# Kernel optimization log

Measured on AMD Instinct MI355X. Metric: run time of the kernel, lower is better.

The kernel has to match this reference:

```python
import jax, jax.numpy as jnp
import numpy as np

B, PTS, D = 8, 4096, 256          # batch, points per sample, hidden_size
QT, QR, QO = 3000, 216, 1         # num_queries: pos bins, 72*3 euler bins, openness


def setup_inputs() -> dict:
    key = jax.random.key(0)
    ks = jax.random.split(key, 11)
    N = B * PTS
    w = lambda k, s: jax.random.normal(k, s, jnp.float32) * 0.02
    return {
        "feat": jax.random.normal(ks[0], (N, D), jnp.float32),
        "npoints_in_batch": jnp.full((B,), PTS, jnp.int32),
        "queries_t": w(ks[1], (QT, D)),
        "Wk_t": w(ks[2], (D, D)),
        "Wv_t": w(ks[3], (D, D)),
        "queries_r": w(ks[4], (QR, D)),
        "Wk_r": w(ks[5], (D, D)),
        "Wv_r": w(ks[6], (D, D)),
        "queries_o": w(ks[7], (QO, D)),
        "Wk_o": w(ks[8], (D, D)),
        "Wv_o": w(ks[9], (D, D)),
    }


def _aggregate(feat, seg, queries, Wk, Wv):
    """Ragged cross-attention pooling + sum over feature dim.

    feat: (N, D) all points; seg: (N,) sample id per point.
    Equivalent to, per sample b: sum_d( softmax_n(q K_b^T/sqrt(D)) V_b )[q, d]
    => (B, Q) since sum over d commutes: attn @ V.sum(-1).
    """
    d = feat.shape[-1]
    k = feat @ Wk                                  # (N, D)
    vsum = (feat @ Wv).sum(-1)                     # (N,)  row-sum of values
    scores = (k @ queries.T) / jnp.sqrt(jnp.float32(d))  # (N, Q)
    m = jax.ops.segment_max(scores, seg, num_segments=B)  # (B, Q)
    e = jnp.exp(scores - m[seg])                   # (N, Q)
    denom = jax.ops.segment_sum(e, seg, num_segments=B)   # (B, Q)
    numer = jax.ops.segment_sum(e * vsum[:, None], seg, num_segments=B)
    return numer / denom                           # (B, Q)


def reference(feat, npoints_in_batch, queries_t, Wk_t, Wv_t,
              queries_r, Wk_r, Wv_r, queries_o, Wk_o, Wv_o):
    N = feat.shape[0]
    seg = jnp.repeat(jnp.arange(B, dtype=jnp.int32), npoints_in_batch,
                     total_repeat_length=N)
    xt = _aggregate(feat, seg, queries_t, Wk_t, Wv_t)  # (B, 3000)
    xr = _aggregate(feat, seg, queries_r, Wk_r, Wv_r)  # (B, 216)
    xo = _aggregate(feat, seg, queries_o, Wk_o, Wv_o)  # (B, 1)
    return (xt, xr, xo)
```

## Files before the change

### kernel.cpp

```cpp
#include <hip/hip_runtime.h>

typedef __attribute__((ext_vector_type(8))) short short8;
typedef __attribute__((ext_vector_type(4))) float f32x4;
typedef unsigned int u32;

#define D_ 256
#define QT_V 3000
#define QR_V 216
#define QO_V 1
#define QPT 3008
#define QPR 224
#define QPO 96
#define QPTOT 3328
#define WQ_TILES 104
#define NSPLIT 16
#define VPAD 32
#define SCALE 0.09016844005556021f
#define TILE_US 8192
#define PSTRIDE 264

__device__ __forceinline__ unsigned short f2bf(float f) {
    union { float f; unsigned int i; } u; u.f = f;
    unsigned int i = u.i + 0x7fffu + ((u.i >> 16) & 1u);
    return (unsigned short)(i >> 16);
}

__device__ __forceinline__ void async_cp16(const unsigned short* g, unsigned short* l) {
    __builtin_amdgcn_global_load_lds((const __attribute__((address_space(1))) u32*)g,
                                     (__attribute__((address_space(3))) u32*)l, 16, 0, 0);
}

__global__ __launch_bounds__(256) void prep(
    const float* __restrict__ feat,
    const float* __restrict__ q_t, const float* __restrict__ q_r,
    const float* __restrict__ q_o,
    const float* __restrict__ wk_t, const float* __restrict__ wk_r,
    const float* __restrict__ wk_o,
    const float* __restrict__ wv_t, const float* __restrict__ wv_r,
    const float* __restrict__ wv_o,
    unsigned short* __restrict__ featb,
    unsigned short* __restrict__ WqT,
    float* __restrict__ vsum,
    int N, int ntiles, int nvs)
{
    __shared__ __align__(16) unsigned short lds[32 * PSTRIDE];
    int blk = blockIdx.x, tid = (int)threadIdx.x;
    int srow = tid >> 3, c8 = tid & 7;
    int wave = tid >> 6, lane = tid & 63;
    int col16 = lane & 15, quad = lane >> 4;

    if (blk < ntiles) {
        int t = blk;
        int row = t * 32 + srow;
        bool valid = row < N;
#pragma unroll
        for (int i = 0; i < 8; ++i) {
            int col = i * 32 + c8 * 4;
            float4 v;
            if (valid) v = *(const float4*)(feat + (size_t)row * D_ + col);
            else { v.x = v.y = v.z = v.w = 0.f; }
            ushort4 o;
            o.x = f2bf(v.x); o.y = f2bf(v.y); o.z = f2bf(v.z); o.w = f2bf(v.w);
            *(ushort4*)(lds + srow * PSTRIDE + col) = o;
        }
        __syncthreads();
#pragma unroll
        for (int i = 0; i < 4; ++i) {
            int cmb = wave * 4 + i;
            int kk = cmb >> 1, sub = cmb & 1;
            short8 v = *(const short8*)(lds + (sub * 16 + col16) * PSTRIDE
                                        + quad * 8 + kk * 32);
            *(short8*)(featb + (size_t)t * TILE_US + cmb * 512 + lane * 8) = v;
        }
    } else if (blk < ntiles + WQ_TILES) {
        int wq = blk - ntiles;
        const float* Q; const float* Wh; int nvalid, lq0, outrow;
        if (wq < 94)       { Q = q_t; Wh = wk_t; nvalid = QT_V; lq0 = wq * 32;         outrow = lq0; }
        else if (wq < 101) { Q = q_r; Wh = wk_r; nvalid = QR_V; lq0 = (wq - 94) * 32;  outrow = QPT + lq0; }
        else               { Q = q_o; Wh = wk_o; nvalid = QO_V; lq0 = (wq - 101) * 32; outrow = QPT + QPR + lq0; }
        int row = lq0 + srow;
        bool valid = row < nvalid;
#pragma unroll
        for (int i = 0; i < 8; ++i) {
            int col = i * 32 + c8 * 4;
            float4 v;
            if (valid) v = *(const float4*)(Q + (size_t)row * D_ + col);
            else { v.x = v.y = v.z = v.w = 0.f; }
            ushort4 o;
            o.x = f2bf(v.x); o.y = f2bf(v.y); o.z = f2bf(v.z); o.w = f2bf(v.w);
            *(ushort4*)(lds + srow * PSTRIDE + col) = o;
        }
        __syncthreads();
        int c0 = wave * 64;
        f32x4 acc[2][4];
#pragma unroll
        for (int mt = 0; mt < 2; ++mt)
#pragma unroll
            for (int nt = 0; nt < 4; ++nt)
                acc[mt][nt] = f32x4{0.f, 0.f, 0.f, 0.f};
#pragma unroll
        for (int kk = 0; kk < 8; ++kk) {
            short8 a0 = *(const short8*)(lds + col16 * PSTRIDE + quad * 8 + kk * 32);
            short8 a1 = *(const short8*)(lds + (16 + col16) * PSTRIDE + quad * 8 + kk * 32);
#pragma unroll
            for (int nt = 0; nt < 4; ++nt) {
                const float* wr = Wh + (size_t)(c0 + nt * 16 + col16) * D_ + quad * 8 + kk * 32;
                float4 x = *(const float4*)(wr);
                float4 y = *(const float4*)(wr + 4);
                short8 bf;
                bf[0] = (short)f2bf(x.x); bf[1] = (short)f2bf(x.y);
                bf[2] = (short)f2bf(x.z); bf[3] = (short)f2bf(x.w);
                bf[4] = (short)f2bf(y.x); bf[5] = (short)f2bf(y.y);
                bf[6] = (short)f2bf(y.z); bf[7] = (short)f2bf(y.w);
                acc[0][nt] = __builtin_amdgcn_mfma_f32_16x16x32_bf16(a0, bf, acc[0][nt], 0, 0, 0);
                acc[1][nt] = __builtin_amdgcn_mfma_f32_16x16x32_bf16(a1, bf, acc[1][nt], 0, 0, 0);
            }
        }
#pragma unroll
        for (int mt = 0; mt < 2; ++mt)
#pragma unroll
            for (int nt = 0; nt < 4; ++nt)
#pragma unroll
                for (int r = 0; r < 4; ++r) {
                    int orow = outrow + mt * 16 + quad * 4 + r;
                    int ocol = c0 + nt * 16 + col16;
                    WqT[(size_t)orow * D_ + ocol] = f2bf(acc[mt][nt][r] * SCALE);
                }
    } else {
        int v = blk - ntiles - WQ_TILES;
        float* wv = (float*)lds;
        for (int f0 = wave * 4; f0 < 768; f0 += 16) {
            int f = f0 + (lane >> 4);
            int hh = f >> 8, c = f & 255;
            const float* base = ((hh == 0) ? wv_t : (hh == 1) ? wv_r : wv_o)
                                + (size_t)c * D_;
            float s = 0.f;
#pragma unroll
            for (int p = 0; p < 4; ++p) {
                float4 x = *(const float4*)(base + p * 64 + (lane & 15) * 4);
                s += x.x + x.y + x.z + x.w;
            }
            s += __shfl_xor(s, 1); s += __shfl_xor(s, 2);
            s += __shfl_xor(s, 4); s += __shfl_xor(s, 8);
            if ((lane & 15) == 0) wv[f] = s;
        }
        __syncthreads();
        int r0 = v * 128;
#pragma unroll 1
        for (int pass = 0; pass < 32; ++pass) {
            int row = r0 + pass * 4 + wave;
            if (row < N) {
                float4 fv = *(const float4*)(feat + (size_t)row * D_ + lane * 4);
                float4 w0 = *(const float4*)(wv + lane * 4);
                float4 w1 = *(const float4*)(wv + 256 + lane * 4);
                float4 w2 = *(const float4*)(wv + 512 + lane * 4);
                float p0 = fv.x * w0.x + fv.y * w0.y + fv.z * w0.z + fv.w * w0.w;
                float p1 = fv.x * w1.x + fv.y * w1.y + fv.z * w1.z + fv.w * w1.w;
                float p2 = fv.x * w2.x + fv.y * w2.y + fv.z * w2.z + fv.w * w2.w;
#pragma unroll
                for (int off = 32; off >= 1; off >>= 1) {
                    p0 += __shfl_xor(p0, off);
                    p1 += __shfl_xor(p1, off);
                    p2 += __shfl_xor(p2, off);
                }
                if (lane == 0) {
                    vsum[0 * (size_t)(N + VPAD) + row] = p0;
                    vsum[1 * (size_t)(N + VPAD) + row] = p1;
                    vsum[2 * (size_t)(N + VPAD) + row] = p2;
                }
            }
        }
        if (v == nvs - 1 && tid < 3 * VPAD) {
            int hh = tid / VPAD, i = tid % VPAD;
            vsum[(size_t)hh * (N + VPAD) + N + i] = 0.f;
        }
    }
}

__global__ __launch_bounds__(256, 4) void attn_main(
    const unsigned short* __restrict__ featb,
    const int* __restrict__ npts,
    const unsigned short* __restrict__ WqT,
    const float* __restrict__ vsum,
    float* __restrict__ partials, int N)
{
    __shared__ __align__(16) unsigned short lds[2][TILE_US];
    int b = blockIdx.z, qblock = blockIdx.y, chunk = blockIdx.x;
    int tid = (int)threadIdx.x;
    int wave = tid >> 6, lane = tid & 63;
    int col = lane & 15, quad = lane >> 4;

    int qp0 = qblock * 128 + wave * 32;
    int h = (qp0 < QPT) ? 0 : ((qp0 < QPT + QPR) ? 1 : 2);
    const float* vs = vsum + (size_t)h * (N + VPAD);

    int start = 0;
#pragma unroll 1
    for (int i = 0; i < b; ++i) start += npts[i];
    int end = start + npts[b];
    if (end > N) end = N;
    if (start < 0) start = 0;
    if (start > end) start = end;
    int bt0 = start >> 5, bt1 = (end + 31) >> 5;
    int ntc = (bt1 - bt0 + NSPLIT - 1) / NSPLIT;
    int ta = bt0 + chunk * ntc;
    int tb = ta + ntc; if (tb > bt1) tb = bt1;

    short8 bfrag[2][8];
#pragma unroll
    for (int qt = 0; qt < 2; ++qt) {
        const unsigned short* wr = WqT + (size_t)(qp0 + qt * 16 + col) * D_ + quad * 8;
#pragma unroll
        for (int kk = 0; kk < 8; ++kk)
            bfrag[qt][kk] = *(const short8*)(wr + kk * 32);
    }

    float den0 = 0.f, num0 = 0.f, den1 = 0.f, num1 = 0.f;
    int p = 0;
    if (ta < tb) {
        const unsigned short* g = featb + (size_t)ta * TILE_US + (wave * 4) * 512 + lane * 8;
#pragma unroll
        for (int i = 0; i < 4; ++i)
            async_cp16(g + i * 512, &lds[0][(wave * 4 + i) * 512]);
    }
#pragma unroll 1
    for (int t = ta; t < tb; ++t) {
        __syncthreads();
        if (t + 1 < tb) {
            const unsigned short* g = featb + (size_t)(t + 1) * TILE_US + (wave * 4) * 512 + lane * 8;
#pragma unroll
            for (int i = 0; i < 4; ++i)
                async_cp16(g + i * 512, &lds[p ^ 1][(wave * 4 + i) * 512]);
        }
        const unsigned short* lp = lds[p];
        f32x4 acc00 = {0.f,0.f,0.f,0.f}, acc01 = {0.f,0.f,0.f,0.f};
        f32x4 acc10 = {0.f,0.f,0.f,0.f}, acc11 = {0.f,0.f,0.f,0.f};
#pragma unroll
        for (int kk = 0; kk < 8; ++kk) {
            short8 a0 = *(const short8*)(lp + (kk * 2 + 0) * 512 + lane * 8);
            short8 a1 = *(const short8*)(lp + (kk * 2 + 1) * 512 + lane * 8);
            acc00 = __builtin_amdgcn_mfma_f32_16x16x32_bf16(a0, bfrag[0][kk], acc00, 0, 0, 0);
            acc10 = __builtin_amdgcn_mfma_f32_16x16x32_bf16(a0, bfrag[1][kk], acc10, 0, 0, 0);
            acc01 = __builtin_amdgcn_mfma_f32_16x16x32_bf16(a1, bfrag[0][kk], acc01, 0, 0, 0);
            acc11 = __builtin_amdgcn_mfma_f32_16x16x32_bf16(a1, bfrag[1][kk], acc11, 0, 0, 0);
        }
        int rb = t * 32 + quad * 4;
        f32x4 v0 = *(const f32x4*)(vs + rb);
        f32x4 v1 = *(const f32x4*)(vs + rb + 16);
        int r0 = t * 32;
        if (r0 >= start && r0 + 32 <= end) {
#pragma unroll
            for (int r = 0; r < 4; ++r) {
                float e00 = __builtin_amdgcn_exp2f(acc00[r]);
                float e01 = __builtin_amdgcn_exp2f(acc01[r]);
                float e10 = __builtin_amdgcn_exp2f(acc10[r]);
                float e11 = __builtin_amdgcn_exp2f(acc11[r]);
                den0 += e00 + e01; num0 += e00 * v0[r] + e01 * v1[r];
                den1 += e10 + e11; num1 += e10 * v0[r] + e11 * v1[r];
            }
        } else {
#pragma unroll
            for (int r = 0; r < 4; ++r) {
                int ra = rb + r, rb2 = rb + 16 + r;
                bool ma = (ra >= start) && (ra < end);
                bool mb = (rb2 >= start) && (rb2 < end);
                float e00 = ma ? __builtin_amdgcn_exp2f(acc00[r]) : 0.f;
                float e01 = mb ? __builtin_amdgcn_exp2f(acc01[r]) : 0.f;
                float e10 = ma ? __builtin_amdgcn_exp2f(acc10[r]) : 0.f;
                float e11 = mb ? __builtin_amdgcn_exp2f(acc11[r]) : 0.f;
                den0 += e00 + e01; num0 += e00 * v0[r] + e01 * v1[r];
                den1 += e10 + e11; num1 += e10 * v0[r] + e11 * v1[r];
            }
        }
        p ^= 1;
    }

    den0 += __shfl_xor(den0, 16); den0 += __shfl_xor(den0, 32);
    num0 += __shfl_xor(num0, 16); num0 += __shfl_xor(num0, 32);
    den1 += __shfl_xor(den1, 16); den1 += __shfl_xor(den1, 32);
    num1 += __shfl_xor(num1, 16); num1 += __shfl_xor(num1, 32);

    if (quad == 0) {
        size_t base = ((size_t)b * QPTOT + (qp0 + col)) * NSPLIT + chunk;
        partials[base * 2]     = den0;
        partials[base * 2 + 1] = num0;
        size_t base1 = base + (size_t)16 * NSPLIT;
        partials[base1 * 2]     = den1;
        partials[base1 * 2 + 1] = num1;
    }
}

__global__ __launch_bounds__(256) void combine_k(
    const float* __restrict__ partials,
    float* __restrict__ out, int Bn)
{
    int gid = blockIdx.x * 256 + threadIdx.x;
    int total = Bn * QPTOT;
    if (gid >= total) return;
    int b = gid / QPTOT, qp = gid - b * QPTOT;
    const float* p = partials + (size_t)gid * NSPLIT * 2;
    float den = 0.f, num = 0.f;
#pragma unroll
    for (int c = 0; c < NSPLIT; ++c) { den += p[c * 2]; num += p[c * 2 + 1]; }
    float val = (den > 0.f) ? (num / den) : 0.f;
    int oidx = -1;
    if (qp < QPT) {
        if (qp < QT_V) oidx = b * QT_V + qp;
    } else if (qp < QPT + QPR) {
        int q = qp - QPT;
        if (q < QR_V) oidx = Bn * QT_V + b * QR_V + q;
    } else {
        int q = qp - QPT - QPR;
        if (q < QO_V) oidx = Bn * (QT_V + QR_V) + b;
    }
    if (oidx >= 0) out[oidx] = val;
}

extern "C" void kernel_launch(void* const* d_in, const int* in_sizes, int n_in,
                              void* d_out, int out_size, void* d_ws, size_t ws_size,
                              hipStream_t stream)
{
    const float* feat = (const float*)d_in[0];
    const int* npts   = (const int*)d_in[1];
    const float* q_t  = (const float*)d_in[2];
    const float* wk_t = (const float*)d_in[3];
    const float* wv_t = (const float*)d_in[4];
    const float* q_r  = (const float*)d_in[5];
    const float* wk_r = (const float*)d_in[6];
    const float* wv_r = (const float*)d_in[7];
    const float* q_o  = (const float*)d_in[8];
    const float* wk_o = (const float*)d_in[9];
    const float* wv_o = (const float*)d_in[10];

    int N  = in_sizes[0] / D_;
    int Bn = in_sizes[1];
    int ntiles = (N + 31) / 32;
    int nvs = (N + 127) / 128;

    char* ws = (char*)d_ws;
    size_t off = 0;
    unsigned short* WqT = (unsigned short*)(ws + off);
    off += (size_t)QPTOT * D_ * sizeof(unsigned short);
    off = (off + 255) & ~(size_t)255;
    unsigned short* featb = (unsigned short*)(ws + off);
    off += (size_t)ntiles * TILE_US * sizeof(unsigned short);
    off = (off + 255) & ~(size_t)255;
    float* vsum = (float*)(ws + off);
    off += (size_t)3 * (N + VPAD) * sizeof(float);
    off = (off + 255) & ~(size_t)255;
    float* partials = (float*)(ws + off);
    off += (size_t)Bn * QPTOT * NSPLIT * 2 * sizeof(float);
    (void)ws_size;

    prep<<<ntiles + WQ_TILES + nvs, 256, 0, stream>>>(
        feat, q_t, q_r, q_o, wk_t, wk_r, wk_o, wv_t, wv_r, wv_o,
        featb, WqT, vsum, N, ntiles, nvs);

    dim3 grid(NSPLIT, QPTOT / 128, Bn);
    attn_main<<<grid, 256, 0, stream>>>(featb, npts, WqT, vsum, partials, N);

    int total = Bn * QPTOT;
    combine_k<<<(total + 255) / 256, 256, 0, stream>>>(partials, (float*)d_out, Bn);
}
```

Baseline: 208.7 us.

## Fuse prep, attention and combine into one persistent cooperative kernel

Merges the three launches into a single cooperative persistent kernel of 1024 blocks that separates its phases with grid syncs and takes work items from atomic counters. The vsum computation is folded into the feature bf16 conversion tile loop, so feat is read once in prep instead of twice. If the cooperative launch fails, the code falls back to four phased launches. The aim is to remove launch gaps and the redundant feat read, at the cost of grid-sync overhead and dynamic scheduling through atomics, and the occupancy of 4 blocks per CU must hold for the cooperative launch to succeed.

Measured after the change: 572.0 us. 2.74x slower.

```diff
diff --git a/kernel.cpp b/kernel.cpp
--- a/kernel.cpp
+++ b/kernel.cpp
@@ -1,4 +1,7 @@
 #include <hip/hip_runtime.h>
+#include <hip/hip_cooperative_groups.h>
+
+namespace cg = cooperative_groups;
 
 typedef __attribute__((ext_vector_type(8))) short short8;
 typedef __attribute__((ext_vector_type(4))) float f32x4;
@@ -12,12 +15,14 @@
 #define QPR 224
 #define QPO 96
 #define QPTOT 3328
+#define NQB 26
 #define WQ_TILES 104
 #define NSPLIT 16
 #define VPAD 32
 #define SCALE 0.09016844005556021f
 #define TILE_US 8192
 #define PSTRIDE 264
+#define GRIDB 1024
 
 __device__ __forceinline__ unsigned short f2bf(float f) {
     union { float f; unsigned int i; } u; u.f = f;
@@ -30,290 +35,300 @@
                                      (__attribute__((address_space(3))) u32*)l, 16, 0, 0);
 }
 
-__global__ __launch_bounds__(256) void prep(
-    const float* __restrict__ feat,
+__global__ __launch_bounds__(256, 4) void fused(
+    const float* __restrict__ feat, const int* __restrict__ npts,
     const float* __restrict__ q_t, const float* __restrict__ q_r,
     const float* __restrict__ q_o,
     const float* __restrict__ wk_t, const float* __restrict__ wk_r,
     const float* __restrict__ wk_o,
     const float* __restrict__ wv_t, const float* __restrict__ wv_r,
     const float* __restrict__ wv_o,
-    unsigned short* __restrict__ featb,
-    unsigned short* __restrict__ WqT,
-    float* __restrict__ vsum,
-    int N, int ntiles, int nvs)
+    unsigned short* __restrict__ featb, unsigned short* __restrict__ WqT,
+    float* __restrict__ wvsum, float* __restrict__ vsum,
+    float* __restrict__ partials, u32* __restrict__ ctr,
+    float* __restrict__ out,
+    int N, int ntiles, int Bn, int phase)
 {
-    __shared__ __align__(16) unsigned short lds[32 * PSTRIDE];
+    __shared__ __align__(16) unsigned short lds[2][TILE_US];
+    __shared__ int wi_sh;
+    unsigned short* plds = &lds[0][0];
+    cg::grid_group gg = cg::this_grid();
+    bool fm = (phase < 0);
+
     int blk = blockIdx.x, tid = (int)threadIdx.x;
     int srow = tid >> 3, c8 = tid & 7;
     int wave = tid >> 6, lane = tid & 63;
     int col16 = lane & 15, quad = lane >> 4;
 
-    if (blk < ntiles) {
-        int t = blk;
-        int row = t * 32 + srow;
-        bool valid = row < N;
-#pragma unroll
-        for (int i = 0; i < 8; ++i) {
-            int col = i * 32 + c8 * 4;
-            float4 v;
-            if (valid) v = *(const float4*)(feat + (size_t)row * D_ + col);
-            else { v.x = v.y = v.z = v.w = 0.f; }
-            ushort4 o;
-            o.x = f2bf(v.x); o.y = f2bf(v.y); o.z = f2bf(v.z); o.w = f2bf(v.w);
-            *(ushort4*)(lds + srow * PSTRIDE + col) = o;
-        }
-        __syncthreads();
-#pragma unroll
-        for (int i = 0; i < 4; ++i) {
-            int cmb = wave * 4 + i;
-            int kk = cmb >> 1, sub = cmb & 1;
-            short8 v = *(const short8*)(lds + (sub * 16 + col16) * PSTRIDE
-                                        + quad * 8 + kk * 32);
-            *(short8*)(featb + (size_t)t * TILE_US + cmb * 512 + lane * 8) = v;
-        }
-    } else if (blk < ntiles + WQ_TILES) {
-        int wq = blk - ntiles;
-        const float* Q; const float* Wh; int nvalid, lq0, outrow;
-        if (wq < 94)       { Q = q_t; Wh = wk_t; nvalid = QT_V; lq0 = wq * 32;         outrow = lq0; }
-        else if (wq < 101) { Q = q_r; Wh = wk_r; nvalid = QR_V; lq0 = (wq - 94) * 32;  outrow = QPT + lq0; }
-        else               { Q = q_o; Wh = wk_o; nvalid = QO_V; lq0 = (wq - 101) * 32; outrow = QPT + QPR + lq0; }
-        int row = lq0 + srow;
-        bool valid = row < nvalid;
-#pragma unroll
-        for (int i = 0; i < 8; ++i) {
-            int col = i * 32 + c8 * 4;
-            float4 v;
-            if (valid) v = *(const float4*)(Q + (size_t)row * D_ + col);
-            else { v.x = v.y = v.z = v.w = 0.f; }
-            ushort4 o;
-            o.x = f2bf(v.x); o.y = f2bf(v.y); o.z = f2bf(v.z); o.w = f2bf(v.w);
-            *(ushort4*)(lds + srow * PSTRIDE + col) = o;
-        }
-        __syncthreads();
-        int c0 = wave * 64;
-        f32x4 acc[2][4];
-#pragma unroll
-        for (int mt = 0; mt < 2; ++mt)
-#pragma unroll
-            for (int nt = 0; nt < 4; ++nt)
-                acc[mt][nt] = f32x4{0.f, 0.f, 0.f, 0.f};
-#pragma unroll
-        for (int kk = 0; kk < 8; ++kk) {
-            short8 a0 = *(const short8*)(lds + col16 * PSTRIDE + quad * 8 + kk * 32);
-            short8 a1 = *(const short8*)(lds + (16 + col16) * PSTRIDE + quad * 8 + kk * 32);
-#pragma unroll
-            for (int nt = 0; nt < 4; ++nt) {
-                const float* wr = Wh + (size_t)(c0 + nt * 16 + col16) * D_ + quad * 8 + kk * 32;
-                float4 x = *(const float4*)(wr);
-                float4 y = *(const float4*)(wr + 4);
-                short8 bf;
-                bf[0] = (short)f2bf(x.x); bf[1] = (short)f2bf(x.y);
-                bf[2] = (short)f2bf(x.z); bf[3] = (short)f2bf(x.w);
-                bf[4] = (short)f2bf(y.x); bf[5] = (short)f2bf(y.y);
-                bf[6] = (short)f2bf(y.z); bf[7] = (short)f2bf(y.w);
-                acc[0][nt] = __builtin_amdgcn_mfma_f32_16x16x32_bf16(a0, bf, acc[0][nt], 0, 0, 0);
-                acc[1][nt] = __builtin_amdgcn_mfma_f32_16x16x32_bf16(a1, bf, acc[1][nt], 0, 0, 0);
-            }
-        }
-#pragma unroll
-        for (int mt = 0; mt < 2; ++mt)
-#pragma unroll
-            for (int nt = 0; nt < 4; ++nt)
-#pragma unroll
-                for (int r = 0; r < 4; ++r) {
-                    int orow = outrow + mt * 16 + quad * 4 + r;
-                    int ocol = c0 + nt * 16 + col16;
-                    WqT[(size_t)orow * D_ + ocol] = f2bf(acc[mt][nt][r] * SCALE);
-                }
-    } else {
-        int v = blk - ntiles - WQ_TILES;
-        float* wv = (float*)lds;
-        for (int f0 = wave * 4; f0 < 768; f0 += 16) {
-            int f = f0 + (lane >> 4);
-            int hh = f >> 8, c = f & 255;
-            const float* base = ((hh == 0) ? wv_t : (hh == 1) ? wv_r : wv_o)
-                                + (size_t)c * D_;
-            float s = 0.f;
-#pragma unroll
-            for (int p = 0; p < 4; ++p) {
-                float4 x = *(const float4*)(base + p * 64 + (lane & 15) * 4);
-                s += x.x + x.y + x.z + x.w;
-            }
-            s += __shfl_xor(s, 1); s += __shfl_xor(s, 2);
-            s += __shfl_xor(s, 4); s += __shfl_xor(s, 8);
-            if ((lane & 15) == 0) wv[f] = s;
-        }
-        __syncthreads();
-        int r0 = v * 128;
-#pragma unroll 1
-        for (int pass = 0; pass < 32; ++pass) {
-            int row = r0 + pass * 4 + wave;
-            if (row < N) {
-                float4 fv = *(const float4*)(feat + (size_t)row * D_ + lane * 4);
-                float4 w0 = *(const float4*)(wv + lane * 4);
-                float4 w1 = *(const float4*)(wv + 256 + lane * 4);
-                float4 w2 = *(const float4*)(wv + 512 + lane * 4);
-                float p0 = fv.x * w0.x + fv.y * w0.y + fv.z * w0.z + fv.w * w0.w;
-                float p1 = fv.x * w1.x + fv.y * w1.y + fv.z * w1.z + fv.w * w1.w;
-                float p2 = fv.x * w2.x + fv.y * w2.y + fv.z * w2.z + fv.w * w2.w;
-#pragma unroll
-                for (int off = 32; off >= 1; off >>= 1) {
-                    p0 += __shfl_xor(p0, off);
-                    p1 += __shfl_xor(p1, off);
-                    p2 += __shfl_xor(p2, off);
-                }
-                if (lane == 0) {
+    if (fm || phase == 0) {
+        if (blk < 3) {
+            const float* Wv = (blk == 0) ? wv_t : ((blk == 1) ? wv_r : wv_o);
+            for (int f0 = wave * 4; f0 < 256; f0 += 16) {
+                int f = f0 + (lane >> 4);
+                const float* base = Wv + (size_t)f * D_;
+                float s = 0.f;
+#pragma unroll
+                for (int p = 0; p < 4; ++p) {
+                    float4 x = *(const float4*)(base + p * 64 + (lane & 15) * 4);
+                    s += x.x + x.y + x.z + x.w;
+                }
+                s += __shfl_xor(s, 1); s += __shfl_xor(s, 2);
+                s += __shfl_xor(s, 4); s += __shfl_xor(s, 8);
+                if ((lane & 15) == 0) wvsum[blk * 256 + f] = s;
+            }
+        } else if (blk == 3) {
+            if (tid < 2) ctr[tid] = 0u;
+            if (tid < 3 * VPAD) {
+                int hh = tid / VPAD, i = tid % VPAD;
+                vsum[(size_t)hh * (N + VPAD) + N + i] = 0.f;
+            }
+        }
+    }
+    if (fm) gg.sync();
+
+    if (fm || phase == 1) {
+        int totB = ntiles + WQ_TILES;
+        for (;;) {
+            if (tid == 0) wi_sh = (int)atomicAdd(&ctr[0], 1u);
+            __syncthreads();
+            int wi = wi_sh;
+            __syncthreads();
+            if (wi >= totB) break;
+            if (wi < ntiles) {
+                int t = wi;
+                int row = t * 32 + srow;
+                bool valid = row < N;
+                float p0 = 0.f, p1 = 0.f, p2 = 0.f;
+#pragma unroll
+                for (int i = 0; i < 8; ++i) {
+                    int col = i * 32 + c8 * 4;
+                    float4 v;
+                    if (valid) v = *(const float4*)(feat + (size_t)row * D_ + col);
+                    else { v.x = v.y = v.z = v.w = 0.f; }
+                    ushort4 o;
+                    o.x = f2bf(v.x); o.y = f2bf(v.y); o.z = f2bf(v.z); o.w = f2bf(v.w);
+                    *(ushort4*)(plds + srow * PSTRIDE + col) = o;
+                    float4 w0 = *(const float4*)(wvsum + col);
+                    float4 w1 = *(const float4*)(wvsum + 256 + col);
+                    float4 w2 = *(const float4*)(wvsum + 512 + col);
+                    p0 += v.x * w0.x + v.y * w0.y + v.z * w0.z + v.w * w0.w;
+                    p1 += v.x * w1.x + v.y * w1.y + v.z * w1.z + v.w * w1.w;
+                    p2 += v.x * w2.x + v.y * w2.y + v.z * w2.z + v.w * w2.w;
+                }
+                p0 += __shfl_xor(p0, 1); p0 += __shfl_xor(p0, 2); p0 += __shfl_xor(p0, 4);
+                p1 += __shfl_xor(p1, 1); p1 += __shfl_xor(p1, 2); p1 += __shfl_xor(p1, 4);
+                p2 += __shfl_xor(p2, 1); p2 += __shfl_xor(p2, 2); p2 += __shfl_xor(p2, 4);
+                if (c8 == 0 && valid) {
                     vsum[0 * (size_t)(N + VPAD) + row] = p0;
                     vsum[1 * (size_t)(N + VPAD) + row] = p1;
                     vsum[2 * (size_t)(N + VPAD) + row] = p2;
                 }
-            }
-        }
-        if (v == nvs - 1 && tid < 3 * VPAD) {
-            int hh = tid / VPAD, i = tid % VPAD;
-            vsum[(size_t)hh * (N + VPAD) + N + i] = 0.f;
-        }
-    }
-}
-
-__global__ __launch_bounds__(256, 4) void attn_main(
-    const unsigned short* __restrict__ featb,
-    const int* __restrict__ npts,
-    const unsigned short* __restrict__ WqT,
-    const float* __restrict__ vsum,
-    float* __restrict__ partials, int N)
-{
-    __shared__ __align__(16) unsigned short lds[2][TILE_US];
-    int b = blockIdx.z, qblock = blockIdx.y, chunk = blockIdx.x;
-    int tid = (int)threadIdx.x;
-    int wave = tid >> 6, lane = tid & 63;
-    int col = lane & 15, quad = lane >> 4;
-
-    int qp0 = qblock * 128 + wave * 32;
-    int h = (qp0 < QPT) ? 0 : ((qp0 < QPT + QPR) ? 1 : 2);
-    const float* vs = vsum + (size_t)h * (N + VPAD);
-
-    int start = 0;
+                __syncthreads();
+#pragma unroll
+                for (int i = 0; i < 4; ++i) {
+                    int cmb = wave * 4 + i;
+                    int kk = cmb >> 1, sub = cmb & 1;
+                    short8 v = *(const short8*)(plds + (sub * 16 + col16) * PSTRIDE
+                                                + quad * 8 + kk * 32);
+                    *(short8*)(featb + (size_t)t * TILE_US + cmb * 512 + lane * 8) = v;
+                }
+            } else {
+                int wq = wi - ntiles;
+                const float* Q; const float* Wh; int nvalid, lq0, outrow;
+                if (wq < 94)       { Q = q_t; Wh = wk_t; nvalid = QT_V; lq0 = wq * 32;         outrow = lq0; }
+                else if (wq < 101) { Q = q_r; Wh = wk_r; nvalid = QR_V; lq0 = (wq - 94) * 32;  outrow = QPT + lq0; }
+                else               { Q = q_o; Wh = wk_o; nvalid = QO_V; lq0 = (wq - 101) * 32; outrow = QPT + QPR + lq0; }
+                int row = lq0 + srow;
+                bool valid = row < nvalid;
+#pragma unroll
+                for (int i = 0; i < 8; ++i) {
+                    int col = i * 32 + c8 * 4;
+                    float4 v;
+                    if (valid) v = *(const float4*)(Q + (size_t)row * D_ + col);
+                    else { v.x = v.y = v.z = v.w = 0.f; }
+                    ushort4 o;
+                    o.x = f2bf(v.x); o.y = f2bf(v.y); o.z = f2bf(v.z); o.w = f2bf(v.w);
+                    *(ushort4*)(plds + srow * PSTRIDE + col) = o;
+                }
+                __syncthreads();
+                int c0 = wave * 64;
+                f32x4 acc[2][4];
+#pragma unroll
+                for (int mt = 0; mt < 2; ++mt)
+#pragma unroll
+                    for (int nt = 0; nt < 4; ++nt)
+                        acc[mt][nt] = f32x4{0.f, 0.f, 0.f, 0.f};
+#pragma unroll
+                for (int kk = 0; kk < 8; ++kk) {
+                    short8 a0 = *(const short8*)(plds + col16 * PSTRIDE + quad * 8 + kk * 32);
+                    short8 a1 = *(const short8*)(plds + (16 + col16) * PSTRIDE + quad * 8 + kk * 32);
+#pragma unroll
+                    for (int nt = 0; nt < 4; ++nt) {
+                        const float* wr = Wh + (size_t)(c0 + nt * 16 + col16) * D_ + quad * 8 + kk * 32;
+                        float4 x = *(const float4*)(wr);
+                        float4 y = *(const float4*)(wr + 4);
+                        short8 bf;
+                        bf[0] = (short)f2bf(x.x); bf[1] = (short)f2bf(x.y);
+                        bf[2] = (short)f2bf(x.z); bf[3] = (short)f2bf(x.w);
+                        bf[4] = (short)f2bf(y.x); bf[5] = (short)f2bf(y.y);
+                        bf[6] = (short)f2bf(y.z); bf[7] = (short)f2bf(y.w);
+                        acc[0][nt] = __builtin_amdgcn_mfma_f32_16x16x32_bf16(a0, bf, acc[0][nt], 0, 0, 0);
+                        acc[1][nt] = __builtin_amdgcn_mfma_f32_16x16x32_bf16(a1, bf, acc[1][nt], 0, 0, 0);
+                    }
+                }
+#pragma unroll
+                for (int mt = 0; mt < 2; ++mt)
+#pragma unroll
+                    for (int nt = 0; nt < 4; ++nt)
+#pragma unroll
+                        for (int r = 0; r < 4; ++r) {
+                            int orow = outrow + mt * 16 + quad * 4 + r;
+                            int ocol = c0 + nt * 16 + col16;
+                            WqT[(size_t)orow * D_ + ocol] = f2bf(acc[mt][nt][r] * SCALE);
+                        }
+            }
+        }
+    }
+    if (fm) gg.sync();
+
+    if (fm || phase == 2) {
+        int totC = NSPLIT * NQB * Bn;
+        for (;;) {
+            if (tid == 0) wi_sh = (int)atomicAdd(&ctr[1], 1u);
+            __syncthreads();
+            int wi = wi_sh;
+            __syncthreads();
+            if (wi >= totC) break;
+            int qblock = wi % NQB;
+            int t2 = wi / NQB;
+            int chunk = t2 % NSPLIT;
+            int b = t2 / NSPLIT;
+
+            int qp0 = qblock * 128 + wave * 32;
+            int h = (qp0 < QPT) ? 0 : ((qp0 < QPT + QPR) ? 1 : 2);
+            const float* vs = vsum + (size_t)h * (N + VPAD);
+
+            int start = 0;
 #pragma unroll 1
-    for (int i = 0; i < b; ++i) start += npts[i];
-    int end = start + npts[b];
-    if (end > N) end = N;
-    if (start < 0) start = 0;
-    if (start > end) start = end;
-    int bt0 = start >> 5, bt1 = (end + 31) >> 5;
-    int ntc = (bt1 - bt0 + NSPLIT - 1) / NSPLIT;
-    int ta = bt0 + chunk * ntc;
-    int tb = ta + ntc; if (tb > bt1) tb = bt1;
-
-    short8 bfrag[2][8];
-#pragma unroll
-    for (int qt = 0; qt < 2; ++qt) {
-        const unsigned short* wr = WqT + (size_t)(qp0 + qt * 16 + col) * D_ + quad * 8;
-#pragma unroll
-        for (int kk = 0; kk < 8; ++kk)
-            bfrag[qt][kk] = *(const short8*)(wr + kk * 32);
-    }
-
-    float den0 = 0.f, num0 = 0.f, den1 = 0.f, num1 = 0.f;
-    int p = 0;
-    if (ta < tb) {
-        const unsigned short* g = featb + (size_t)ta * TILE_US + (wave * 4) * 512 + lane * 8;
-#pragma unroll
-        for (int i = 0; i < 4; ++i)
-            async_cp16(g + i * 512, &lds[0][(wave * 4 + i) * 512]);
-    }
+            for (int i = 0; i < b; ++i) start += npts[i];
+            int end = start + npts[b];
+            if (end > N) end = N;
+            if (start < 0) start = 0;
+            if (start > end) start = end;
+            int bt0 = start >> 5, bt1 = (end + 31) >> 5;
+            int ntc = (bt1 - bt0 + NSPLIT - 1) / NSPLIT;
+            int ta = bt0 + chunk * ntc;
+            int tb = ta + ntc; if (tb > bt1) tb = bt1;
+
+            short8 bfrag[2][8];
+#pragma unroll
+            for (int qt = 0; qt < 2; ++qt) {
+                const unsigned short* wr = WqT + (size_t)(qp0 + qt * 16 + col16) * D_ + quad * 8;
+#pragma unroll
+                for (int kk = 0; kk < 8; ++kk)
+                    bfrag[qt][kk] = *(const short8*)(wr + kk * 32);
+            }
+
+            float den0 = 0.f, num0 = 0.f, den1 = 0.f, num1 = 0.f;
+            int p = 0;
+            if (ta < tb) {
+                const unsigned short* g = featb + (size_t)ta * TILE_US + (wave * 4) * 512 + lane * 8;
+#pragma unroll
+                for (int i = 0; i < 4; ++i)
+                    async_cp16(g + i * 512, &lds[0][(wave * 4 + i) * 512]);
+            }
 #pragma unroll 1
-    for (int t = ta; t < tb; ++t) {
-        __syncthreads();
-        if (t + 1 < tb) {
-            const unsigned short* g = featb + (size_t)(t + 1) * TILE_US + (wave * 4) * 512 + lane * 8;
-#pragma unroll
-            for (int i = 0; i < 4; ++i)
-                async_cp16(g + i * 512, &lds[p ^ 1][(wave * 4 + i) * 512]);
-        }
-        const unsigned short* lp = lds[p];
-        f32x4 acc00 = {0.f,0.f,0.f,0.f}, acc01 = {0.f,0.f,0.f,0.f};
-        f32x4 acc10 = {0.f,0.f,0.f,0.f}, acc11 = {0.f,0.f,0.f,0.f};
-#pragma unroll
-        for (int kk = 0; kk < 8; ++kk) {
-            short8 a0 = *(const short8*)(lp + (kk * 2 + 0) * 512 + lane * 8);
-            short8 a1 = *(const short8*)(lp + (kk * 2 + 1) * 512 + lane * 8);
-            acc00 = __builtin_amdgcn_mfma_f32_16x16x32_bf16(a0, bfrag[0][kk], acc00, 0, 0, 0);
-            acc10 = __builtin_amdgcn_mfma_f32_16x16x32_bf16(a0, bfrag[1][kk], acc10, 0, 0, 0);
-            acc01 = __builtin_amdgcn_mfma_f32_16x16x32_bf16(a1, bfrag[0][kk], acc01, 0, 0, 0);
-            acc11 = __builtin_amdgcn_mfma_f32_16x16x32_bf16(a1, bfrag[1][kk], acc11, 0, 0, 0);
-        }
-        int rb = t * 32 + quad * 4;
-        f32x4 v0 = *(const f32x4*)(vs + rb);
-        f32x4 v1 = *(const f32x4*)(vs + rb + 16);
-        int r0 = t * 32;
-        if (r0 >= start && r0 + 32 <= end) {
-#pragma unroll
-            for (int r = 0; r < 4; ++r) {
-                float e00 = __builtin_amdgcn_exp2f(acc00[r]);
-                float e01 = __builtin_amdgcn_exp2f(acc01[r]);
-                float e10 = __builtin_amdgcn_exp2f(acc10[r]);
-                float e11 = __builtin_amdgcn_exp2f(acc11[r]);
-                den0 += e00 + e01; num0 += e00 * v0[r] + e01 * v1[r];
-                den1 += e10 + e11; num1 += e10 * v0[r] + e11 * v1[r];
-            }
-        } else {
-#pragma unroll
-            for (int r = 0; r < 4; ++r) {
-                int ra = rb + r, rb2 = rb + 16 + r;
-                bool ma = (ra >= start) && (ra < end);
-                bool mb = (rb2 >= start) && (rb2 < end);
-                float e00 = ma ? __builtin_amdgcn_exp2f(acc00[r]) : 0.f;
-                float e01 = mb ? __builtin_amdgcn_exp2f(acc01[r]) : 0.f;
-                float e10 = ma ? __builtin_amdgcn_exp2f(acc10[r]) : 0.f;
-                float e11 = mb ? __builtin_amdgcn_exp2f(acc11[r]) : 0.f;
-                den0 += e00 + e01; num0 += e00 * v0[r] + e01 * v1[r];
-                den1 += e10 + e11; num1 += e10 * v0[r] + e11 * v1[r];
-            }
-        }
-        p ^= 1;
-    }
-
-    den0 += __shfl_xor(den0, 16); den0 += __shfl_xor(den0, 32);
-    num0 += __shfl_xor(num0, 16); num0 += __shfl_xor(num0, 32);
-    den1 += __shfl_xor(den1, 16); den1 += __shfl_xor(den1, 32);
-    num1 += __shfl_xor(num1, 16); num1 += __shfl_xor(num1, 32);
-
-    if (quad == 0) {
-        size_t base = ((size_t)b * QPTOT + (qp0 + col)) * NSPLIT + chunk;
-        partials[base * 2]     = den0;
-        partials[base * 2 + 1] = num0;
-        size_t base1 = base + (size_t)16 * NSPLIT;
-        partials[base1 * 2]     = den1;
-        partials[base1 * 2 + 1] = num1;
-    }
-}
-
-__global__ __launch_bounds__(256) void combine_k(
-    const float* __restrict__ partials,
-    float* __restrict__ out, int Bn)
-{
-    int gid = blockIdx.x * 256 + threadIdx.x;
-    int total = Bn * QPTOT;
-    if (gid >= total) return;
-    int b = gid / QPTOT, qp = gid - b * QPTOT;
-    const float* p = partials + (size_t)gid * NSPLIT * 2;
-    float den = 0.f, num = 0.f;
-#pragma unroll
-    for (int c = 0; c < NSPLIT; ++c) { den += p[c * 2]; num += p[c * 2 + 1]; }
-    float val = (den > 0.f) ? (num / den) : 0.f;
-    int oidx = -1;
-    if (qp < QPT) {
-        if (qp < QT_V) oidx = b * QT_V + qp;
-    } else if (qp < QPT + QPR) {
-        int q = qp - QPT;
-        if (q < QR_V) oidx = Bn * QT_V + b * QR_V + q;
-    } else {
-        int q = qp - QPT - QPR;
-        if (q < QO_V) oidx = Bn * (QT_V + QR_V) + b;
-    }
-    if (oidx >= 0) out[oidx] = val;
+            for (int t = ta; t < tb; ++t) {
+                __syncthreads();
+                if (t + 1 < tb) {
+                    const unsigned short* g = featb + (size_t)(t + 1) * TILE_US + (wave * 4) * 512 + lane * 8;
+#pragma unroll
+                    for (int i = 0; i < 4; ++i)
+                        async_cp16(g + i * 512, &lds[p ^ 1][(wave * 4 + i) * 512]);
+                }
+                const unsigned short* lp = lds[p];
+                f32x4 acc00 = {0.f,0.f,0.f,0.f}, acc01 = {0.f,0.f,0.f,0.f};
+                f32x4 acc10 = {0.f,0.f,0.f,0.f}, acc11 = {0.f,0.f,0.f,0.f};
+#pragma unroll
+                for (int kk = 0; kk < 8; ++kk) {
+                    short8 a0 = *(const short8*)(lp + (kk * 2 + 0) * 512 + lane * 8);
+                    short8 a1 = *(const short8*)(lp + (kk * 2 + 1) * 512 + lane * 8);
+                    acc00 = __builtin_amdgcn_mfma_f32_16x16x32_bf16(a0, bfrag[0][kk], acc00, 0, 0, 0);
+                    acc10 = __builtin_amdgcn_mfma_f32_16x16x32_bf16(a0, bfrag[1][kk], acc10, 0, 0, 0);
+                    acc01 = __builtin_amdgcn_mfma_f32_16x16x32_bf16(a1, bfrag[0][kk], acc01, 0, 0, 0);
+                    acc11 = __builtin_amdgcn_mfma_f32_16x16x32_bf16(a1, bfrag[1][kk], acc11, 0, 0, 0);
+                }
+                int rb = t * 32 + quad * 4;
+                f32x4 v0 = *(const f32x4*)(vs + rb);
+                f32x4 v1 = *(const f32x4*)(vs + rb + 16);
+                int r0 = t * 32;
+                if (r0 >= start && r0 + 32 <= end) {
+#pragma unroll
+                    for (int r = 0; r < 4; ++r) {
+                        float e00 = __builtin_amdgcn_exp2f(acc00[r]);
+                        float e01 = __builtin_amdgcn_exp2f(acc01[r]);
+                        float e10 = __builtin_amdgcn_exp2f(acc10[r]);
+                        float e11 = __builtin_amdgcn_exp2f(acc11[r]);
+                        den0 += e00 + e01; num0 += e00 * v0[r] + e01 * v1[r];
+                        den1 += e10 + e11; num1 += e10 * v0[r] + e11 * v1[r];
+                    }
+                } else {
+#pragma unroll
+                    for (int r = 0; r < 4; ++r) {
+                        int ra = rb + r, rb2 = rb + 16 + r;
+                        bool ma = (ra >= start) && (ra < end);
+                        bool mb = (rb2 >= start) && (rb2 < end);
+                        float e00 = ma ? __builtin_amdgcn_exp2f(acc00[r]) : 0.f;
+                        float e01 = mb ? __builtin_amdgcn_exp2f(acc01[r]) : 0.f;
+                        float e10 = ma ? __builtin_amdgcn_exp2f(acc10[r]) : 0.f;
+                        float e11 = mb ? __builtin_amdgcn_exp2f(acc11[r]) : 0.f;
+                        den0 += e00 + e01; num0 += e00 * v0[r] + e01 * v1[r];
+                        den1 += e10 + e11; num1 += e10 * v0[r] + e11 * v1[r];
+                    }
+                }
+                p ^= 1;
+            }
+
+            den0 += __shfl_xor(den0, 16); den0 += __shfl_xor(den0, 32);
+            num0 += __shfl_xor(num0, 16); num0 += __shfl_xor(num0, 32);
+            den1 += __shfl_xor(den1, 16); den1 += __shfl_xor(den1, 32);
+            num1 += __shfl_xor(num1, 16); num1 += __shfl_xor(num1, 32);
+
+            if (quad == 0) {
+                size_t base = ((size_t)b * QPTOT + (qp0 + col16)) * NSPLIT + chunk;
+                partials[base * 2]     = den0;
+                partials[base * 2 + 1] = num0;
+                size_t base1 = base + (size_t)16 * NSPLIT;
+                partials[base1 * 2]     = den1;
+                partials[base1 * 2 + 1] = num1;
+            }
+        }
+    }
+    if (fm) gg.sync();
+
+    if (fm || phase == 3) {
+        int gid = blk * 256 + tid;
+        int total = Bn * QPTOT;
+        if (gid < total) {
+            int b = gid / QPTOT, qp = gid - b * QPTOT;
+            const float* pp = partials + (size_t)gid * NSPLIT * 2;
+            float den = 0.f, num = 0.f;
+#pragma unroll
+            for (int c = 0; c < NSPLIT; ++c) { den += pp[c * 2]; num += pp[c * 2 + 1]; }
+            float val = (den > 0.f) ? (num / den) : 0.f;
+            int oidx = -1;
+            if (qp < QPT) {
+                if (qp < QT_V) oidx = b * QT_V + qp;
+            } else if (qp < QPT + QPR) {
+                int q = qp - QPT;
+                if (q < QR_V) oidx = Bn * QT_V + b * QR_V + q;
+            } else {
+                int q = qp - QPT - QPR;
+                if (q < QO_V) oidx = Bn * (QT_V + QR_V) + b;
+            }
+            if (oidx >= 0) out[oidx] = val;
+        }
+    }
 }
 
 extern "C" void kernel_launch(void* const* d_in, const int* in_sizes, int n_in,
@@ -335,7 +350,6 @@
     int N  = in_sizes[0] / D_;
     int Bn = in_sizes[1];
     int ntiles = (N + 31) / 32;
-    int nvs = (N + 127) / 128;
 
     char* ws = (char*)d_ws;
     size_t off = 0;
@@ -345,20 +359,40 @@
     unsigned short* featb = (unsigned short*)(ws + off);
     off += (size_t)ntiles * TILE_US * sizeof(unsigned short);
     off = (off + 255) & ~(size_t)255;
+    float* wvsum = (float*)(ws + off);
+    off += 3 * D_ * sizeof(float);
+    off = (off + 255) & ~(size_t)255;
     float* vsum = (float*)(ws + off);
     off += (size_t)3 * (N + VPAD) * sizeof(float);
     off = (off + 255) & ~(size_t)255;
     float* partials = (float*)(ws + off);
     off += (size_t)Bn * QPTOT * NSPLIT * 2 * sizeof(float);
+    off = (off + 255) & ~(size_t)255;
+    u32* ctr = (u32*)(ws + off);
+    off += 2 * sizeof(u32);
     (void)ws_size;
 
-    prep<<<ntiles + WQ_TILES + nvs, 256, 0, stream>>>(
-        feat, q_t, q_r, q_o, wk_t, wk_r, wk_o, wv_t, wv_r, wv_o,
-        featb, WqT, vsum, N, ntiles, nvs);
-
-    dim3 grid(NSPLIT, QPTOT / 128, Bn);
-    attn_main<<<grid, 256, 0, stream>>>(featb, npts, WqT, vsum, partials, N);
-
-    int total = Bn * QPTOT;
-    combine_k<<<(total + 255) / 256, 256, 0, stream>>>(partials, (float*)d_out, Bn);
+    float* outp = (float*)d_out;
+    int phase = -1;
+    void* args[] = {
+        (void*)&feat, (void*)&npts,
+        (void*)&q_t, (void*)&q_r, (void*)&q_o,
+        (void*)&wk_t, (void*)&wk_r, (void*)&wk_o,
+        (void*)&wv_t, (void*)&wv_r, (void*)&wv_o,
+        (void*)&featb, (void*)&WqT,
+        (void*)&wvsum, (void*)&vsum,
+        (void*)&partials, (void*)&ctr,
+        (void*)&outp,
+        (void*)&N, (void*)&ntiles, (void*)&Bn, (void*)&phase
+    };
+    hipError_t e = hipLaunchCooperativeKernel((void*)fused, dim3(GRIDB), dim3(256),
+                                              args, 0, stream);
+    if (e != hipSuccess) {
+        (void)hipGetLastError();
+        for (int ph = 0; ph < 4; ++ph) {
+            fused<<<GRIDB, 256, 0, stream>>>(
+                feat, npts, q_t, q_r, q_o, wk_t, wk_r, wk_o, wv_t, wv_r, wv_o,
+                featb, WqT, wvsum, vsum, partials, ctr, outp, N, ntiles, Bn, ph);
+        }
+    }
 }
```
